# Optimization experiments

Hardware: AMD Instinct MI355X
Metric: run time of the kernel (lower is better)

## Reference

```python
import jax, jax.numpy as jnp
import numpy as np

N_HEAD, D_K = 8, 16

def _ln(x, g, b):
    m = jnp.mean(x, -1, keepdims=True)
    v = jnp.var(x, -1, keepdims=True)
    return (x - m) * jax.lax.rsqrt(v + 1e-5) * g + b

def _enc_layer(x, wq, bq, wk, bk, wv, bv, wo, bo, g1, be1, cw1, cb1, cw2, cb2, g2, be2):
    B, L, D = x.shape
    q = (x @ wq + bq).reshape(B, L, N_HEAD, D_K)
    k = (x @ wk + bk).reshape(B, L, N_HEAD, D_K)
    v = (x @ wv + bv).reshape(B, L, N_HEAD, D_K)
    attn = jnp.einsum('blhd,bmhd->bhlm', q, k) / jnp.sqrt(jnp.float32(D_K))
    attn = jax.nn.softmax(attn, axis=-1)
    o = jnp.einsum('bhlm,bmhd->blhd', attn, v).reshape(B, L, -1)
    x = _ln(o @ wo + bo + x, g1, be1)          # post-LN residual (MHA)
    h = jax.nn.relu(x @ cw1 + cb1)             # 1x1 conv == linear
    return _ln(h @ cw2 + cb2 + x, g2, be2)     # post-LN residual (FFN)

def setup_inputs() -> dict:
    key = jax.random.key(0)
    ks = jax.random.split(key, 20)
    N, D, NNZ = 100000, 128, 2000000
    B, L, NL, DI = 32, 256, 2, 512
    s = 0.02
    inp = {}
    inp['ego'] = jax.random.normal(ks[0], (N, D), jnp.float32)
    inp['vals'] = jax.random.uniform(ks[1], (NNZ,), jnp.float32) / 20.0  # ~normalized adj values
    inp['W1'] = jax.random.normal(ks[2], (D, D), jnp.float32) * s
    inp['b1'] = jnp.zeros((D,), jnp.float32)
    inp['W2'] = jax.random.normal(ks[3], (D, D), jnp.float32) * s
    inp['b2'] = jnp.zeros((D,), jnp.float32)
    inp['enc_in'] = jax.random.normal(ks[4], (B, L, D), jnp.float32)
    inp['wq'] = jax.random.normal(ks[5], (NL, D, D), jnp.float32) * s
    inp['bq'] = jnp.zeros((NL, D), jnp.float32)
    inp['wk'] = jax.random.normal(ks[6], (NL, D, D), jnp.float32) * s
    inp['bk'] = jnp.zeros((NL, D), jnp.float32)
    inp['wv'] = jax.random.normal(ks[7], (NL, D, D), jnp.float32) * s
    inp['bv'] = jnp.zeros((NL, D), jnp.float32)
    inp['wo'] = jax.random.normal(ks[8], (NL, D, D), jnp.float32) * s
    inp['bo'] = jnp.zeros((NL, D), jnp.float32)
    inp['ln1_g'] = jnp.ones((NL, D), jnp.float32)
    inp['ln1_b'] = jnp.zeros((NL, D), jnp.float32)
    inp['cw1'] = jax.random.normal(ks[9], (NL, D, DI), jnp.float32) * s
    inp['cb1'] = jnp.zeros((NL, DI), jnp.float32)
    inp['cw2'] = jax.random.normal(ks[10], (NL, DI, D), jnp.float32) * s
    inp['cb2'] = jnp.zeros((NL, D), jnp.float32)
    inp['ln2_g'] = jnp.ones((NL, D), jnp.float32)
    inp['ln2_b'] = jnp.zeros((NL, D), jnp.float32)
    inp['rows'] = jnp.sort(jax.random.randint(ks[11], (NNZ,), 0, N, jnp.int32))
    inp['cols'] = jax.random.randint(ks[12], (NNZ,), 0, N, jnp.int32)
    return inp

def reference(ego, vals, W1, b1, W2, b2, enc_in, wq, bq, wk, bk, wv, bv, wo, bo,
              ln1_g, ln1_b, cw1, cb1, cw2, cb2, ln2_g, ln2_b, rows, cols):
    N = ego.shape[0]
    # sparse A_in @ ego  (COO SpMM via gather + segment_sum)
    side = jax.ops.segment_sum(vals[:, None] * ego[cols], rows, num_segments=N)
    # bi-interaction aggregator (dropout=identity in eval)
    sum_emb = jax.nn.leaky_relu((ego + side) @ W1 + b1)
    bi_emb = jax.nn.leaky_relu((ego * side) @ W2 + b2)
    agg = sum_emb + bi_emb
    # transformer encoder over edge sequences
    x = enc_in
    for i in range(wq.shape[0]):
        x = _enc_layer(x, wq[i], bq[i], wk[i], bk[i], wv[i], bv[i], wo[i], bo[i],
                       ln1_g[i], ln1_b[i], cw1[i], cb1[i], cw2[i], cb2[i], ln2_g[i], ln2_b[i])
    return (agg, x)
```

## Files before the change

kernel.cpp:

```cpp
#include <hip/hip_runtime.h>

typedef __attribute__((ext_vector_type(8))) short bf16x8;
typedef __attribute__((ext_vector_type(4))) float f32x4;

__device__ __forceinline__ unsigned short f2b(float f) {
    union { float f; unsigned int i; } u; u.f = f;
    return (unsigned short)((u.i + 0x7FFFu + ((u.i >> 16) & 1u)) >> 16);
}
__device__ __forceinline__ unsigned int packbf2(float a, float b) {
    return (unsigned int)f2b(a) | ((unsigned int)f2b(b) << 16);
}

__device__ __forceinline__ void spmm_block(
    const unsigned int* __restrict__ egob, const float* __restrict__ vals,
    const int* __restrict__ rows, const int* __restrict__ cols,
    float* __restrict__ side, int nnz, int blk)
{
    int tid = threadIdx.x;
    int wave = tid >> 6, lane = tid & 63;
    int e0 = blk * 256 + wave * 64;
    if (e0 >= nnz) return;

    int idx = e0 + lane;
    int last = nnz - 1;
    bool ok = idx < nnz;
    int safe = ok ? idx : last;
    int my_row = rows[safe];
    int my_col = cols[safe];
    float my_val = ok ? vals[safe] : 0.f;

    unsigned int pre[16];
    #pragma unroll
    for (int j = 0; j < 16; ++j) {
        unsigned int c = (unsigned int)__builtin_amdgcn_readlane(my_col, j);
        pre[j] = *(egob + ((size_t)c << 6) + lane);
    }

    float ax = 0.f, ay = 0.f;
    int cur = __builtin_amdgcn_readlane(my_row, 0);
    #pragma unroll
    for (int e = 0; e < 64; ++e) {
        int r = __builtin_amdgcn_readlane(my_row, e);
        float vv = __int_as_float(__builtin_amdgcn_readlane(__float_as_int(my_val), e));
        unsigned int u = pre[e & 15];
        if (e < 48) {
            unsigned int c = (unsigned int)__builtin_amdgcn_readlane(my_col, e + 16);
            pre[e & 15] = *(egob + ((size_t)c << 6) + lane);
        }
        if (r != cur) {
            atomicAdd(&side[(size_t)cur * 128 + lane * 2], ax);
            atomicAdd(&side[(size_t)cur * 128 + lane * 2 + 1], ay);
            ax = 0.f; ay = 0.f; cur = r;
        }
        ax = fmaf(vv, __uint_as_float(u << 16), ax);
        ay = fmaf(vv, __uint_as_float(u & 0xFFFF0000u), ay);
    }
    atomicAdd(&side[(size_t)cur * 128 + lane * 2], ax);
    atomicAdd(&side[(size_t)cur * 128 + lane * 2 + 1], ay);
}

#define LDAB 40
#define LDBI 72

__device__ __forceinline__ void gemm2_core(
    const float* __restrict__ A, const float* __restrict__ W,
    const float* __restrict__ bias, const float* __restrict__ R,
    const float* __restrict__ g, const float* __restrict__ bta,
    float* __restrict__ C, int M, int N, int K, int act,
    int bm, int bn, unsigned short* As, unsigned short* Bs,
    float* redS, float* redSS)
{
    int tid = threadIdx.x, wave = tid >> 6, lane = tid & 63;
    int lm = lane & 15, quad = lane >> 4;
    int wm = wave >> 1, wn = wave & 1;

    f32x4 acc[2][4];
    #pragma unroll
    for (int i = 0; i < 2; ++i)
        #pragma unroll
        for (int j = 0; j < 4; ++j) acc[i][j] = (f32x4)(0.f);

    for (int k0 = 0; k0 < K; k0 += 32) {
        {
            int m = tid >> 2, kc = (tid & 3) * 8;
            const float* p = A + (size_t)(bm + m) * K + k0 + kc;
            float4 a0 = *(const float4*)p, a1 = *(const float4*)(p + 4);
            uint4 pk;
            pk.x = packbf2(a0.x, a0.y); pk.y = packbf2(a0.z, a0.w);
            pk.z = packbf2(a1.x, a1.y); pk.w = packbf2(a1.z, a1.w);
            *(uint4*)&As[m * LDAB + kc] = pk;
        }
        {
            int nn = tid & 127, kh = (tid >> 7) * 16;
            const float* p = W + (size_t)(k0 + kh) * N + bn + nn;
            float w[16];
            #pragma unroll
            for (int j = 0; j < 16; ++j) w[j] = p[(size_t)j * N];
            uint4 pk;
            pk.x = packbf2(w[0], w[1]);  pk.y = packbf2(w[2], w[3]);
            pk.z = packbf2(w[4], w[5]);  pk.w = packbf2(w[6], w[7]);
            *(uint4*)&Bs[nn * LDAB + kh] = pk;
            pk.x = packbf2(w[8], w[9]);  pk.y = packbf2(w[10], w[11]);
            pk.z = packbf2(w[12], w[13]); pk.w = packbf2(w[14], w[15]);
            *(uint4*)&Bs[nn * LDAB + kh + 8] = pk;
        }
        __syncthreads();
        bf16x8 af[2], bfr[4];
        #pragma unroll
        for (int mi = 0; mi < 2; ++mi)
            af[mi] = *(bf16x8*)&As[(wm * 32 + mi * 16 + lm) * LDAB + quad * 8];
        #pragma unroll
        for (int ni = 0; ni < 4; ++ni)
            bfr[ni] = *(bf16x8*)&Bs[(wn * 64 + ni * 16 + lm) * LDAB + quad * 8];
        #pragma unroll
        for (int mi = 0; mi < 2; ++mi)
            #pragma unroll
            for (int ni = 0; ni < 4; ++ni)
                acc[mi][ni] = __builtin_amdgcn_mfma_f32_16x16x32_bf16(
                    af[mi], bfr[ni], acc[mi][ni], 0, 0, 0);
        __syncthreads();
    }

    #pragma unroll
    for (int mi = 0; mi < 2; ++mi) {
        #pragma unroll
        for (int r = 0; r < 4; ++r) {
            int row = bm + wm * 32 + mi * 16 + quad * 4 + r;
            #pragma unroll
            for (int ni = 0; ni < 4; ++ni) {
                int col = bn + wn * 64 + ni * 16 + lm;
                float v = acc[mi][ni][r] + bias[col];
                if (R) v += R[(size_t)row * N + col];
                if (act) v = fmaxf(v, 0.f);
                acc[mi][ni][r] = v;
            }
        }
    }

    if (g) {
        #pragma unroll
        for (int mi = 0; mi < 2; ++mi) {
            #pragma unroll
            for (int r = 0; r < 4; ++r) {
                float s = 0.f, ss = 0.f;
                #pragma unroll
                for (int ni = 0; ni < 4; ++ni) {
                    float v = acc[mi][ni][r];
                    s += v; ss = fmaf(v, v, ss);
                }
                #pragma unroll
                for (int off = 1; off < 16; off <<= 1) {
                    s  += __shfl_xor(s, off, 64);
                    ss += __shfl_xor(ss, off, 64);
                }
                if (lm == 0) {
                    int lr = wm * 32 + mi * 16 + quad * 4 + r;
                    redS[wn * 64 + lr] = s;
                    redSS[wn * 64 + lr] = ss;
                }
            }
        }
        __syncthreads();
        #pragma unroll
        for (int mi = 0; mi < 2; ++mi) {
            #pragma unroll
            for (int r = 0; r < 4; ++r) {
                int lr = wm * 32 + mi * 16 + quad * 4 + r;
                int row = bm + lr;
                float s = redS[lr] + redS[64 + lr];
                float ss = redSS[lr] + redSS[64 + lr];
                float mean = s * (1.f / 128.f);
                float var = ss * (1.f / 128.f) - mean * mean;
                float rstd = rsqrtf(var + 1e-5f);
                #pragma unroll
                for (int ni = 0; ni < 4; ++ni) {
                    int col = wn * 64 + ni * 16 + lm;
                    float y = (acc[mi][ni][r] - mean) * rstd * g[col] + bta[col];
                    C[(size_t)row * 128 + col] = y;
                }
            }
        }
    } else {
        #pragma unroll
        for (int mi = 0; mi < 2; ++mi) {
            #pragma unroll
            for (int r = 0; r < 4; ++r) {
                int row = bm + wm * 32 + mi * 16 + quad * 4 + r;
                #pragma unroll
                for (int ni = 0; ni < 4; ++ni) {
                    int col = bn + wn * 64 + ni * 16 + lm;
                    C[(size_t)row * N + col] = acc[mi][ni][r];
                }
            }
        }
    }
}

__device__ __forceinline__ void bi_core3(
    const float* __restrict__ ego, const float* __restrict__ side,
    const unsigned short* __restrict__ W1t, const unsigned short* __restrict__ W2t,
    const float* __restrict__ b1, const float* __restrict__ b2,
    float* __restrict__ out, int M, int bm,
    unsigned short* Us, unsigned short* Ms)
{
    int tid = threadIdx.x, wave = tid >> 6, lane = tid & 63;
    int lm = lane & 15, quad = lane >> 4;
    int wm = wave >> 1, wn = wave & 1;

    f32x4 acc1[2][4], acc2[2][4];
    #pragma unroll
    for (int i = 0; i < 2; ++i)
        #pragma unroll
        for (int j = 0; j < 4; ++j) { acc1[i][j] = (f32x4)(0.f); acc2[i][j] = (f32x4)(0.f); }

    #pragma unroll
    for (int h = 0; h < 2; ++h) {
        int k0 = h * 64;
        if (h) __syncthreads();
        {
            int m = tid >> 2, kc = (tid & 3) * 16;
            int gm = bm + m;
            float e[16], s[16];
            if (gm < M) {
                const float* pe = ego + (size_t)gm * 128 + k0 + kc;
                const float* ps = side + (size_t)gm * 128 + k0 + kc;
                #pragma unroll
                for (int j = 0; j < 4; ++j) {
                    float4 ev = *(const float4*)(pe + j * 4);
                    float4 sv = *(const float4*)(ps + j * 4);
                    e[j*4+0] = ev.x; e[j*4+1] = ev.y; e[j*4+2] = ev.z; e[j*4+3] = ev.w;
                    s[j*4+0] = sv.x; s[j*4+1] = sv.y; s[j*4+2] = sv.z; s[j*4+3] = sv.w;
                }
            } else {
                #pragma unroll
                for (int j = 0; j < 16; ++j) { e[j] = 0.f; s[j] = 0.f; }
            }
            #pragma unroll
            for (int j = 0; j < 2; ++j) {
                int b0 = j * 8;
                uint4 pu, pv;
                pu.x = packbf2(e[b0+0]+s[b0+0], e[b0+1]+s[b0+1]);
                pu.y = packbf2(e[b0+2]+s[b0+2], e[b0+3]+s[b0+3]);
                pu.z = packbf2(e[b0+4]+s[b0+4], e[b0+5]+s[b0+5]);
                pu.w = packbf2(e[b0+6]+s[b0+6], e[b0+7]+s[b0+7]);
                pv.x = packbf2(e[b0+0]*s[b0+0], e[b0+1]*s[b0+1]);
                pv.y = packbf2(e[b0+2]*s[b0+2], e[b0+3]*s[b0+3]);
                pv.z = packbf2(e[b0+4]*s[b0+4], e[b0+5]*s[b0+5]);
                pv.w = packbf2(e[b0+6]*s[b0+6], e[b0+7]*s[b0+7]);
                *(uint4*)&Us[m * LDBI + kc + b0] = pu;
                *(uint4*)&Ms[m * LDBI + kc + b0] = pv;
            }
        }
        __syncthreads();
        #pragma unroll
        for (int ks = 0; ks < 2; ++ks) {
            bf16x8 au[2], am[2], bf1[4], bf2[4];
            #pragma unroll
            for (int mi = 0; mi < 2; ++mi) {
                int off = (wm * 32 + mi * 16 + lm) * LDBI + ks * 32 + quad * 8;
                au[mi] = *(bf16x8*)&Us[off];
                am[mi] = *(bf16x8*)&Ms[off];
            }
            #pragma unroll
            for (int ni = 0; ni < 4; ++ni) {
                size_t n = (size_t)(wn * 64 + ni * 16 + lm);
                size_t koff = n * 128 + k0 + ks * 32 + quad * 8;
                bf1[ni] = *(const bf16x8*)(W1t + koff);
                bf2[ni] = *(const bf16x8*)(W2t + koff);
            }
            #pragma unroll
            for (int mi = 0; mi < 2; ++mi)
                #pragma unroll
                for (int ni = 0; ni < 4; ++ni) {
                    acc1[mi][ni] = __builtin_amdgcn_mfma_f32_16x16x32_bf16(
                        au[mi], bf1[ni], acc1[mi][ni], 0, 0, 0);
                    acc2[mi][ni] = __builtin_amdgcn_mfma_f32_16x16x32_bf16(
                        am[mi], bf2[ni], acc2[mi][ni], 0, 0, 0);
                }
        }
    }
    #pragma unroll
    for (int mi = 0; mi < 2; ++mi) {
        #pragma unroll
        for (int r = 0; r < 4; ++r) {
            int row = bm + wm * 32 + mi * 16 + quad * 4 + r;
            if (row < M) {
                #pragma unroll
                for (int ni = 0; ni < 4; ++ni) {
                    int col = wn * 64 + ni * 16 + lm;
                    float v1 = acc1[mi][ni][r] + b1[col];
                    v1 = v1 > 0.f ? v1 : 0.01f * v1;
                    float v2 = acc2[mi][ni][r] + b2[col];
                    v2 = v2 > 0.f ? v2 : 0.01f * v2;
                    out[(size_t)row * 128 + col] = v1 + v2;
                }
            }
        }
    }
}


__global__ __launch_bounds__(256) void qkv2_pre(
    const float* __restrict__ A,
    const float* __restrict__ wq, const float* __restrict__ wk, const float* __restrict__ wv,
    const float* __restrict__ bq, const float* __restrict__ bk, const float* __restrict__ bv,
    float* __restrict__ Q, float* __restrict__ Ko, float* __restrict__ V, int M, int encGy,
    float* __restrict__ side, int Nn,
    const float* __restrict__ ego, unsigned int* __restrict__ egob,
    const float* __restrict__ W1, const float* __restrict__ W2,
    unsigned short* __restrict__ W1t, unsigned short* __restrict__ W2t,
    int encN, int ZB, int CB, int WTB)
{
    __shared__ unsigned short As[64 * LDAB];
    __shared__ unsigned short Bs[128 * LDAB];
    __shared__ float redS[128], redSS[128];
    int gid = blockIdx.x;
    int tid = threadIdx.x;
    if (gid >= encN) {
        int j = gid - encN;
        if (j < ZB) {
            size_t n4 = (size_t)Nn * 32;
            float4 z = make_float4(0.f, 0.f, 0.f, 0.f);
            for (size_t i = (size_t)j * 256 + tid; i < n4; i += (size_t)ZB * 256)
                ((float4*)side)[i] = z;
        } else if (j < ZB + CB) {
            int c = j - ZB;
            size_t n4 = (size_t)Nn * 32;
            for (size_t i = (size_t)c * 256 + tid; i < n4; i += (size_t)CB * 256) {
                float4 a = *(const float4*)(ego + i * 4);
                uint2 p;
                p.x = packbf2(a.x, a.y);
                p.y = packbf2(a.z, a.w);
                *(uint2*)(egob + i * 2) = p;
            }
        } else {
            int c = j - ZB - CB;
            for (int ch = c * 256 + tid; ch < 4096; ch += WTB * 256) {
                int w = ch >> 11, rem = ch & 2047;
                int n = rem >> 4, k8 = rem & 15;
                const float* src = w ? W2 : W1;
                unsigned short* dst = w ? W2t : W1t;
                float t[8];
                #pragma unroll
                for (int jj = 0; jj < 8; ++jj)
                    t[jj] = src[(size_t)(k8 * 8 + jj) * 128 + n];
                uint4 pk;
                pk.x = packbf2(t[0], t[1]); pk.y = packbf2(t[2], t[3]);
                pk.z = packbf2(t[4], t[5]); pk.w = packbf2(t[6], t[7]);
                *(uint4*)&dst[(size_t)n * 128 + k8 * 8] = pk;
            }
        }
        return;
    }
    int sel = gid / encGy, by = gid % encGy;
    const float* W = (sel == 0) ? wq : (sel == 1) ? wk : wv;
    const float* b = (sel == 0) ? bq : (sel == 1) ? bk : bv;
    float* C = (sel == 0) ? Q : (sel == 1) ? Ko : V;
    gemm2_core(A, W, b, nullptr, nullptr, nullptr, C, M, 128, 128, 0,
               by * 64, 0, As, Bs, redS, redSS);
}

__global__ __launch_bounds__(256) void qkv2_spmm(
    const float* __restrict__ A,
    const float* __restrict__ wq, const float* __restrict__ wk, const float* __restrict__ wv,
    const float* __restrict__ bq, const float* __restrict__ bk, const float* __restrict__ bv,
    float* __restrict__ Q, float* __restrict__ Ko, float* __restrict__ V, int M, int encGy,
    const unsigned int* __restrict__ egob, const float* __restrict__ vals,
    const int* __restrict__ rows, const int* __restrict__ cols,
    float* __restrict__ side, int nnz, int spmmBase, int encN)
{
    __shared__ unsigned short As[64 * LDAB];
    __shared__ unsigned short Bs[128 * LDAB];
    __shared__ float redS[128], redSS[128];
    int gid = blockIdx.x;
    if (gid >= encN) {
        spmm_block(egob, vals, rows, cols, side, nnz, spmmBase + gid - encN);
        return;
    }
    int sel = gid / encGy, by = gid % encGy;
    const float* W = (sel == 0) ? wq : (sel == 1) ? wk : wv;
    const float* b = (sel == 0) ? bq : (sel == 1) ? bk : bv;
    float* C = (sel == 0) ? Q : (sel == 1) ? Ko : V;
    gemm2_core(A, W, b, nullptr, nullptr, nullptr, C, M, 128, 128, 0,
               by * 64, 0, As, Bs, redS, redSS);
}

__global__ __launch_bounds__(256) void gemm2_spmm(
    const float* __restrict__ A, const float* __restrict__ W,
    const float* __restrict__ bias, const float* __restrict__ R,
    const float* __restrict__ g, const float* __restrict__ bta,
    float* __restrict__ C, int M, int N, int K, int act, int encGy,
    const unsigned int* __restrict__ egob, const float* __restrict__ vals,
    const int* __restrict__ rows, const int* __restrict__ cols,
    float* __restrict__ side, int nnz, int spmmBase, int encN)
{
    __shared__ unsigned short As[64 * LDAB];
    __shared__ unsigned short Bs[128 * LDAB];
    __shared__ float redS[128], redSS[128];
    int gid = blockIdx.x;
    if (gid >= encN) {
        spmm_block(egob, vals, rows, cols, side, nnz, spmmBase + gid - encN);
        return;
    }
    int bx = gid / encGy, by = gid % encGy;
    gemm2_core(A, W, bias, R, g, bta, C, M, N, K, act,
               by * 64, bx * 128, As, Bs, redS, redSS);
}

__global__ __launch_bounds__(256) void gemm2_bi3(
    const float* __restrict__ A, const float* __restrict__ W,
    const float* __restrict__ bias, const float* __restrict__ R,
    const float* __restrict__ g, const float* __restrict__ bta,
    float* __restrict__ C, int M, int N, int K, int act, int encGy, int encN,
    const float* __restrict__ ego, const float* __restrict__ side,
    const unsigned short* __restrict__ W1t, const unsigned short* __restrict__ W2t,
    const float* __restrict__ b1, const float* __restrict__ b2,
    float* __restrict__ out, int Mbi, int biBase)
{
    __shared__ char smem[18432];
    int gid = blockIdx.x;
    if (gid < encN) {
        unsigned short* As = (unsigned short*)smem;
        unsigned short* Bs = (unsigned short*)(smem + 5120);
        float* redS  = (float*)(smem + 15360);
        float* redSS = (float*)(smem + 15360 + 512);
        int bx = gid / encGy, by = gid % encGy;
        gemm2_core(A, W, bias, R, g, bta, C, M, N, K, act,
                   by * 64, bx * 128, As, Bs, redS, redSS);
    } else {
        int bb = biBase + (gid - encN);
        unsigned short* Us = (unsigned short*)smem;
        unsigned short* Ms = (unsigned short*)(smem + 9216);
        bi_core3(ego, side, W1t, W2t, b1, b2, out, Mbi, bb * 64, Us, Ms);
    }
}

__device__ __forceinline__ void attn_block(
    const float* __restrict__ q, const float* __restrict__ k,
    const float* __restrict__ v, float* __restrict__ o, int NH,
    int bh, float* Ks, float* Vs)
{
    const int L = 256, DK = 16;
    int b = bh / NH, h = bh % NH;
    int tid = threadIdx.x;

    size_t qbase = ((size_t)(b * L + tid) * NH + h) * DK;
    float qr[16];
    #pragma unroll
    for (int d4 = 0; d4 < 4; ++d4) {
        float4 t = *(const float4*)(q + qbase + d4 * 4);
        qr[d4*4+0] = t.x * 0.25f; qr[d4*4+1] = t.y * 0.25f;
        qr[d4*4+2] = t.z * 0.25f; qr[d4*4+3] = t.w * 0.25f;
    }
    float acc[16];
    #pragma unroll
    for (int d = 0; d < 16; ++d) acc[d] = 0.f;
    float mmax = -1e30f, ssum = 0.f;

    for (int c0 = 0; c0 < L; c0 += 128) {
        __syncthreads();
        for (int i = tid; i < 128 * 4; i += 256) {
            int ll = i >> 2, d4 = (i & 3) * 4;
            size_t gg = ((size_t)(b * L + c0 + ll) * NH + h) * DK + d4;
            *(float4*)&Ks[ll * 16 + d4] = *(const float4*)(k + gg);
            *(float4*)&Vs[ll * 16 + d4] = *(const float4*)(v + gg);
        }
        __syncthreads();

        for (int kk = 0; kk < 128; ++kk) {
            float dot = 0.f;
            #pragma unroll
            for (int d4 = 0; d4 < 4; ++d4) {
                float4 kv = *(const float4*)&Ks[kk * 16 + d4 * 4];
                dot = fmaf(qr[d4*4+0], kv.x, dot);
                dot = fmaf(qr[d4*4+1], kv.y, dot);
                dot = fmaf(qr[d4*4+2], kv.z, dot);
                dot = fmaf(qr[d4*4+3], kv.w, dot);
            }
            if (dot > mmax) {
                float alpha = __expf(mmax - dot);
                ssum *= alpha;
                #pragma unroll
                for (int d = 0; d < 16; ++d) acc[d] *= alpha;
                mmax = dot;
            }
            float p = __expf(dot - mmax);
            ssum += p;
            #pragma unroll
            for (int d4 = 0; d4 < 4; ++d4) {
                float4 vv = *(const float4*)&Vs[kk * 16 + d4 * 4];
                acc[d4*4+0] = fmaf(p, vv.x, acc[d4*4+0]);
                acc[d4*4+1] = fmaf(p, vv.y, acc[d4*4+1]);
                acc[d4*4+2] = fmaf(p, vv.z, acc[d4*4+2]);
                acc[d4*4+3] = fmaf(p, vv.w, acc[d4*4+3]);
            }
        }
    }
    float inv = 1.f / ssum;
    #pragma unroll
    for (int d4 = 0; d4 < 4; ++d4) {
        float4 t;
        t.x = acc[d4*4+0] * inv; t.y = acc[d4*4+1] * inv;
        t.z = acc[d4*4+2] * inv; t.w = acc[d4*4+3] * inv;
        *(float4*)(o + qbase + d4 * 4) = t;
    }
}

__global__ __launch_bounds__(256) void attn_spmm(
    const float* __restrict__ q, const float* __restrict__ k,
    const float* __restrict__ v, float* __restrict__ o, int NH,
    const unsigned int* __restrict__ egob, const float* __restrict__ vals,
    const int* __restrict__ rows, const int* __restrict__ cols,
    float* __restrict__ side, int nnz, int spmmBase, int encN)
{
    __shared__ float Ks[128 * 16];
    __shared__ float Vs[128 * 16];
    int gid = blockIdx.x;
    if (gid >= encN) {
        spmm_block(egob, vals, rows, cols, side, nnz, spmmBase + gid - encN);
        return;
    }
    attn_block(q, k, v, o, NH, gid, Ks, Vs);
}

extern "C" void kernel_launch(void* const* d_in, const int* in_sizes, int n_in,
                              void* d_out, int out_size, void* d_ws, size_t ws_size,
                              hipStream_t stream) {
    const float* ego    = (const float*)d_in[0];
    const float* vals   = (const float*)d_in[1];
    const float* W1     = (const float*)d_in[2];
    const float* b1     = (const float*)d_in[3];
    const float* W2     = (const float*)d_in[4];
    const float* b2     = (const float*)d_in[5];
    const float* enc_in = (const float*)d_in[6];
    const float* wq  = (const float*)d_in[7];
    const float* bq  = (const float*)d_in[8];
    const float* wk  = (const float*)d_in[9];
    const float* bk  = (const float*)d_in[10];
    const float* wv  = (const float*)d_in[11];
    const float* bv  = (const float*)d_in[12];
    const float* wo  = (const float*)d_in[13];
    const float* bo  = (const float*)d_in[14];
    const float* ln1_g = (const float*)d_in[15];
    const float* ln1_b = (const float*)d_in[16];
    const float* cw1 = (const float*)d_in[17];
    const float* cb1 = (const float*)d_in[18];
    const float* cw2 = (const float*)d_in[19];
    const float* cb2 = (const float*)d_in[20];
    const float* ln2_g = (const float*)d_in[21];
    const float* ln2_b = (const float*)d_in[22];
    const int* rows = (const int*)d_in[23];
    const int* cols = (const int*)d_in[24];

    const int D = 128, DI = 512, NH = 8, L = 256;
    const int Nn   = in_sizes[0] / D;
    const int nnz  = in_sizes[1];
    const int NL   = in_sizes[7] / (D * D);
    const int Menc = in_sizes[6] / D;
    const int Bb   = Menc / L;

    float* ws = (float*)d_ws;
    size_t off = 0;
    float* side = ws + off; off += (size_t)Nn * D;
    float* Qb = ws + off; off += (size_t)Menc * D;
    float* Kb = ws + off; off += (size_t)Menc * D;
    float* Vb = ws + off; off += (size_t)Menc * D;
    float* Ob = ws + off; off += (size_t)Menc * D;
    float* XA = ws + off; off += (size_t)Menc * D;
    float* XB = ws + off; off += (size_t)Menc * D;
    float* Hb = ws + off; off += (size_t)Menc * DI;
    unsigned int* egob = (unsigned int*)(ws + off); off += (size_t)Nn * (D / 2);
    unsigned short* W1t = (unsigned short*)(ws + off); off += (size_t)D * D / 2;
    unsigned short* W2t = (unsigned short*)(ws + off); off += (size_t)D * D / 2;

    float* outAgg = (float*)d_out;
    float* outX   = (float*)d_out + (size_t)Nn * D;

    const int spmmBlocks = (nnz + 255) / 256;
    const int nSpmmStages = 5 * NL - 3;
    const int perS = (spmmBlocks + nSpmmStages - 1) / nSpmmStages;
    const int biTiles = (Nn + 63) / 64;
    const int perB = (biTiles + 1) / 2;
    const int biStart = 5 * NL - 1;
    const int encGy = Menc / 64;
    const int ZB = 512, CB = 1024, WTB = 16;
    int sidx = 0, sci = 0, bci = 0;

    const float* x = enc_in;
    for (int i = 0; i < NL; ++i) {
        const size_t wOff = (size_t)i * D * D;
        int base, cnt;
        #define SPMM_CHUNK base = sci * perS; cnt = spmmBlocks - base; \
                           if (cnt < 0) cnt = 0; if (cnt > perS) cnt = perS; sci++
        #define BI_CHUNK   base = bci * perB; cnt = biTiles - base; \
                           if (cnt < 0) cnt = 0; if (cnt > perB) cnt = perB; bci++

        sidx++;
        if (sidx == 1) {
            qkv2_pre<<<3 * encGy + ZB + CB + WTB, 256, 0, stream>>>(
                x, wq + wOff, wk + wOff, wv + wOff,
                bq + (size_t)i * D, bk + (size_t)i * D, bv + (size_t)i * D,
                Qb, Kb, Vb, Menc, encGy,
                side, Nn, ego, egob, W1, W2, W1t, W2t, 3 * encGy, ZB, CB, WTB);
        } else {
            SPMM_CHUNK;
            qkv2_spmm<<<3 * encGy + cnt, 256, 0, stream>>>(
                x, wq + wOff, wk + wOff, wv + wOff,
                bq + (size_t)i * D, bk + (size_t)i * D, bv + (size_t)i * D,
                Qb, Kb, Vb, Menc, encGy,
                egob, vals, rows, cols, side, nnz, base, 3 * encGy);
        }

        sidx++;
        SPMM_CHUNK;
        attn_spmm<<<Bb * NH + cnt, 256, 0, stream>>>(
            Qb, Kb, Vb, Ob, NH,
            egob, vals, rows, cols, side, nnz, base, Bb * NH);

        sidx++;
        SPMM_CHUNK;
        gemm2_spmm<<<encGy + cnt, 256, 0, stream>>>(
            Ob, wo + wOff, bo + (size_t)i * D, x,
            ln1_g + (size_t)i * D, ln1_b + (size_t)i * D, XA, Menc, D, D, 0, encGy,
            egob, vals, rows, cols, side, nnz, base, encGy);

        sidx++;
        if (sidx >= biStart) {
            BI_CHUNK;
            gemm2_bi3<<<4 * encGy + cnt, 256, 0, stream>>>(
                XA, cw1 + (size_t)i * D * DI, cb1 + (size_t)i * DI, nullptr,
                nullptr, nullptr, Hb, Menc, DI, D, 1, encGy, 4 * encGy,
                ego, side, W1t, W2t, b1, b2, outAgg, Nn, base);
        } else {
            SPMM_CHUNK;
            gemm2_spmm<<<4 * encGy + cnt, 256, 0, stream>>>(
                XA, cw1 + (size_t)i * D * DI, cb1 + (size_t)i * DI, nullptr,
                nullptr, nullptr, Hb, Menc, DI, D, 1, encGy,
                egob, vals, rows, cols, side, nnz, base, 4 * encGy);
        }

        sidx++;
        float* dst = (i == NL - 1) ? outX : XB;
        if (sidx >= biStart) {
            BI_CHUNK;
            gemm2_bi3<<<encGy + cnt, 256, 0, stream>>>(
                Hb, cw2 + (size_t)i * DI * D, cb2 + (size_t)i * D, XA,
                ln2_g + (size_t)i * D, ln2_b + (size_t)i * D, dst, Menc, D, DI, 0,
                encGy, encGy,
                ego, side, W1t, W2t, b1, b2, outAgg, Nn, base);
        } else {
            SPMM_CHUNK;
            gemm2_spmm<<<encGy + cnt, 256, 0, stream>>>(
                Hb, cw2 + (size_t)i * DI * D, cb2 + (size_t)i * D, XA,
                ln2_g + (size_t)i * D, ln2_b + (size_t)i * D, dst, Menc, D, DI, 0, encGy,
                egob, vals, rows, cols, side, nnz, base, encGy);
        }
        #undef SPMM_CHUNK
        #undef BI_CHUNK
        x = XB;
    }
}
```

Measured before the change: 481.9 us.

## Split attention queries across four threads and four blocks per head

Each (batch, head) attention block is split into four blocks of 64 queries. Four threads now share each query, each scanning an interleaved quarter of the keys, and their online-softmax states are merged with wave shuffles at the end. This cuts the long serial key loop per thread and quadruples the attention grid, so the GPU has more parallel work. In exchange, K and V are loaded into LDS four times per head, the merge step adds shuffle work, and the LDS row stride is padded to 18 floats to reduce bank conflicts. That padding makes the float4 LDS reads not 16-byte aligned, which may cost extra or split accesses.

After: 845.8 us. +75.5%, slower.

```diff
diff --git a/kernel.cpp b/kernel.cpp
--- a/kernel.cpp
+++ b/kernel.cpp
@@ -61,6 +61,7 @@
 
 #define LDAB 40
 #define LDBI 72
+#define LDKV 18
 
 __device__ __forceinline__ void gemm2_core(
     const float* __restrict__ A, const float* __restrict__ W,
@@ -295,6 +296,99 @@
                     out[(size_t)row * 128 + col] = v1 + v2;
                 }
             }
+        }
+    }
+}
+
+__device__ __forceinline__ void attn_block(
+    const float* __restrict__ q, const float* __restrict__ k,
+    const float* __restrict__ v, float* __restrict__ o, int NH,
+    int blk, float* Ks, float* Vs)
+{
+    const int L = 256, DK = 16;
+    int bh = blk >> 2, qq = blk & 3;
+    int b = bh / NH, h = bh % NH;
+    int tid = threadIdx.x;
+    int qi = tid >> 2, seg = tid & 3;
+
+    int lq = qq * 64 + qi;
+    size_t qbase = ((size_t)(b * L + lq) * NH + h) * DK;
+    float qr[16];
+    #pragma unroll
+    for (int d4 = 0; d4 < 4; ++d4) {
+        float4 t = *(const float4*)(q + qbase + d4 * 4);
+        qr[d4*4+0] = t.x * 0.25f; qr[d4*4+1] = t.y * 0.25f;
+        qr[d4*4+2] = t.z * 0.25f; qr[d4*4+3] = t.w * 0.25f;
+    }
+    float acc[16];
+    #pragma unroll
+    for (int d = 0; d < 16; ++d) acc[d] = 0.f;
+    float mmax = -1e30f, ssum = 0.f;
+
+    for (int c0 = 0; c0 < L; c0 += 128) {
+        __syncthreads();
+        for (int i = tid; i < 128 * 4; i += 256) {
+            int ll = i >> 2, d4 = (i & 3) * 4;
+            size_t gg = ((size_t)(b * L + c0 + ll) * NH + h) * DK + d4;
+            *(float4*)&Ks[ll * LDKV + d4] = *(const float4*)(k + gg);
+            *(float4*)&Vs[ll * LDKV + d4] = *(const float4*)(v + gg);
+        }
+        __syncthreads();
+
+        for (int i = 0; i < 32; ++i) {
+            int kk = (i << 2) | seg;
+            const float* kr = &Ks[kk * LDKV];
+            float dot = 0.f;
+            #pragma unroll
+            for (int d4 = 0; d4 < 4; ++d4) {
+                float4 kv = *(const float4*)&kr[d4 * 4];
+                dot = fmaf(qr[d4*4+0], kv.x, dot);
+                dot = fmaf(qr[d4*4+1], kv.y, dot);
+                dot = fmaf(qr[d4*4+2], kv.z, dot);
+                dot = fmaf(qr[d4*4+3], kv.w, dot);
+            }
+            if (dot > mmax) {
+                float alpha = __expf(mmax - dot);
+                ssum *= alpha;
+                #pragma unroll
+                for (int d = 0; d < 16; ++d) acc[d] *= alpha;
+                mmax = dot;
+            }
+            float p = __expf(dot - mmax);
+            ssum += p;
+            const float* vr = &Vs[kk * LDKV];
+            #pragma unroll
+            for (int d4 = 0; d4 < 4; ++d4) {
+                float4 vv = *(const float4*)&vr[d4 * 4];
+                acc[d4*4+0] = fmaf(p, vv.x, acc[d4*4+0]);
+                acc[d4*4+1] = fmaf(p, vv.y, acc[d4*4+1]);
+                acc[d4*4+2] = fmaf(p, vv.z, acc[d4*4+2]);
+                acc[d4*4+3] = fmaf(p, vv.w, acc[d4*4+3]);
+            }
+        }
+    }
+
+    float m1 = fmaxf(mmax, __shfl_xor(mmax, 1, 64));
+    float m2 = fmaxf(m1, __shfl_xor(m1, 2, 64));
+    float f = __expf(mmax - m2);
+    float sl = ssum * f;
+    sl += __shfl_xor(sl, 1, 64);
+    sl += __shfl_xor(sl, 2, 64);
+    #pragma unroll
+    for (int d = 0; d < 16; ++d) {
+        float a = acc[d] * f;
+        a += __shfl_xor(a, 1, 64);
+        a += __shfl_xor(a, 2, 64);
+        acc[d] = a;
+    }
+    if (seg == 0) {
+        float inv = 1.f / sl;
+        #pragma unroll
+        for (int d4 = 0; d4 < 4; ++d4) {
+            float4 t;
+            t.x = acc[d4*4+0] * inv; t.y = acc[d4*4+1] * inv;
+            t.z = acc[d4*4+2] * inv; t.w = acc[d4*4+3] * inv;
+            *(float4*)(o + qbase + d4 * 4) = t;
         }
     }
 }
@@ -435,77 +529,6 @@
     }
 }
 
-__device__ __forceinline__ void attn_block(
-    const float* __restrict__ q, const float* __restrict__ k,
-    const float* __restrict__ v, float* __restrict__ o, int NH,
-    int bh, float* Ks, float* Vs)
-{
-    const int L = 256, DK = 16;
-    int b = bh / NH, h = bh % NH;
-    int tid = threadIdx.x;
-
-    size_t qbase = ((size_t)(b * L + tid) * NH + h) * DK;
-    float qr[16];
-    #pragma unroll
-    for (int d4 = 0; d4 < 4; ++d4) {
-        float4 t = *(const float4*)(q + qbase + d4 * 4);
-        qr[d4*4+0] = t.x * 0.25f; qr[d4*4+1] = t.y * 0.25f;
-        qr[d4*4+2] = t.z * 0.25f; qr[d4*4+3] = t.w * 0.25f;
-    }
-    float acc[16];
-    #pragma unroll
-    for (int d = 0; d < 16; ++d) acc[d] = 0.f;
-    float mmax = -1e30f, ssum = 0.f;
-
-    for (int c0 = 0; c0 < L; c0 += 128) {
-        __syncthreads();
-        for (int i = tid; i < 128 * 4; i += 256) {
-            int ll = i >> 2, d4 = (i & 3) * 4;
-            size_t gg = ((size_t)(b * L + c0 + ll) * NH + h) * DK + d4;
-            *(float4*)&Ks[ll * 16 + d4] = *(const float4*)(k + gg);
-            *(float4*)&Vs[ll * 16 + d4] = *(const float4*)(v + gg);
-        }
-        __syncthreads();
-
-        for (int kk = 0; kk < 128; ++kk) {
-            float dot = 0.f;
-            #pragma unroll
-            for (int d4 = 0; d4 < 4; ++d4) {
-                float4 kv = *(const float4*)&Ks[kk * 16 + d4 * 4];
-                dot = fmaf(qr[d4*4+0], kv.x, dot);
-                dot = fmaf(qr[d4*4+1], kv.y, dot);
-                dot = fmaf(qr[d4*4+2], kv.z, dot);
-                dot = fmaf(qr[d4*4+3], kv.w, dot);
-            }
-            if (dot > mmax) {
-                float alpha = __expf(mmax - dot);
-                ssum *= alpha;
-                #pragma unroll
-                for (int d = 0; d < 16; ++d) acc[d] *= alpha;
-                mmax = dot;
-            }
-            float p = __expf(dot - mmax);
-            ssum += p;
-            #pragma unroll
-            for (int d4 = 0; d4 < 4; ++d4) {
-                float4 vv = *(const float4*)&Vs[kk * 16 + d4 * 4];
-                acc[d4*4+0] = fmaf(p, vv.x, acc[d4*4+0]);
-                acc[d4*4+1] = fmaf(p, vv.y, acc[d4*4+1]);
-                acc[d4*4+2] = fmaf(p, vv.z, acc[d4*4+2]);
-                acc[d4*4+3] = fmaf(p, vv.w, acc[d4*4+3]);
-            }
-        }
-    }
-    float inv = 1.f / ssum;
-    #pragma unroll
-    for (int d4 = 0; d4 < 4; ++d4) {
-        float4 t;
-        t.x = acc[d4*4+0] * inv; t.y = acc[d4*4+1] * inv;
-        t.z = acc[d4*4+2] * inv; t.w = acc[d4*4+3] * inv;
-        *(float4*)(o + qbase + d4 * 4) = t;
-    }
-}
-
 __global__ __launch_bounds__(256) void attn_spmm(
     const float* __restrict__ q, const float* __restrict__ k,
     const float* __restrict__ v, float* __restrict__ o, int NH,
@@ -513,8 +536,8 @@
     const int* __restrict__ rows, const int* __restrict__ cols,
     float* __restrict__ side, int nnz, int spmmBase, int encN)
 {
-    __shared__ float Ks[128 * 16];
-    __shared__ float Vs[128 * 16];
+    __shared__ float Ks[128 * LDKV];
+    __shared__ float Vs[128 * LDKV];
     int gid = blockIdx.x;
     if (gid >= encN) {
         spmm_block(egob, vals, rows, cols, side, nnz, spmmBase + gid - encN);
@@ -613,9 +636,9 @@
 
         sidx++;
         SPMM_CHUNK;
-        attn_spmm<<<Bb * NH + cnt, 256, 0, stream>>>(
+        attn_spmm<<<Bb * NH * 4 + cnt, 256, 0, stream>>>(
             Qb, Kb, Vb, Ob, NH,
-            egob, vals, rows, cols, side, nnz, base, Bb * NH);
+            egob, vals, rows, cols, side, nnz, base, Bb * NH * 4);
 
         sidx++;
         SPMM_CHUNK;
```
